# Kernel optimization log

Measured on AMD Instinct MI355X. Metric: run time of the kernel, lower is better.

Reference implementation:

```python
import jax, jax.numpy as jnp
import numpy as np

B, L, A, F = 4096, 12, 768, 4096  # batch, n_layers, d_activations, d_features


def setup_inputs() -> dict:
    key = jax.random.key(0)
    k_x, k_enc, k_dec, k_m, k_s = jax.random.split(key, 5)
    x = jax.random.normal(k_x, (B, L, A), dtype=jnp.float32)
    # Encoder: uniform(-1/sqrt(F), 1/sqrt(F)) per reset_parameters
    enc_thresh = 1.0 / np.sqrt(F)
    W_enc = jax.random.uniform(k_enc, (L, A, F), jnp.float32, -enc_thresh, enc_thresh)
    # Decoder: triangular weights W_i of shape (i+1, F, A), packed along axis 0.
    # Total rows = L*(L+1)//2. uniform(-1/sqrt(A*L), 1/sqrt(A*L)).
    dec_thresh = 1.0 / np.sqrt(A * L)
    n_tri = L * (L + 1) // 2
    W_dec_packed = jax.random.uniform(k_dec, (n_tri, F, A), jnp.float32, -dec_thresh, dec_thresh)
    # JumpReLU threshold per (layer, feature), init 0.03
    theta = jnp.full((L, F), 0.03, dtype=jnp.float32)
    # Dimensionwise input standardizer stats (per layer, per activation dim)
    in_mean = 0.1 * jax.random.normal(k_m, (L, A), dtype=jnp.float32)
    in_std = 1.0 + 0.1 * jax.random.uniform(k_s, (L, A), dtype=jnp.float32)
    return {"x": x, "in_mean": in_mean, "in_std": in_std, "W_enc": W_enc,
            "theta": theta, "W_dec_packed": W_dec_packed}


def reference(x, in_mean, in_std, W_enc, theta, W_dec_packed):
    # Input standardization: (x - mean) / std, broadcast over batch
    sx = (x - in_mean[None]) / in_std[None]                      # [B, L, A]
    # Encoder: per-layer dense projection
    enc = jnp.einsum('bla,laf->blf', sx, W_enc)                  # [B, L, F]
    # JumpReLU: x * (x > theta)
    act = enc * (enc > theta[None]).astype(enc.dtype)            # [B, L, F]
    # Decoder: triangular accumulation. Layer i reads features of layers 0..i
    # with its own weight tensor W_i (slice of the packed triangular buffer).
    n_layers = W_enc.shape[0]
    preds = []
    off = 0
    for i in range(n_layers):
        W_i = W_dec_packed[off:off + i + 1]                      # [i+1, F, A]
        preds.append(jnp.einsum('blf,lfa->ba', act[:, :i + 1], W_i))
        off += i + 1
    logits = jnp.stack(preds, axis=1)                            # [B, L, A]
    # Original forward returns (logits, encoder_out, concat_w_dec); the
    # concat_w_dec list is just a reshape of the decoder params, omitted here.
    return logits, enc
```

## Files before the change

kernel.cpp:

```cpp
#include <hip/hip_runtime.h>
#include <cstdint>
#include <cstddef>

#define B_ 4096
#define L_ 12
#define A_ 768
#define F_ 4096
#define NTRI 78

typedef __bf16 bf16x8 __attribute__((ext_vector_type(8)));
typedef float f32x4 __attribute__((ext_vector_type(4)));
typedef unsigned short u16x4 __attribute__((ext_vector_type(4)));
typedef unsigned short u16x8 __attribute__((ext_vector_type(8)));

__device__ __forceinline__ unsigned short f32_to_bf16(float f) {
  unsigned int u = __float_as_uint(f);
  u += 0x7fffu + ((u >> 16) & 1u);
  return (unsigned short)(u >> 16);
}

__device__ __forceinline__ void gload_lds16(const void* g, void* l) {
  __builtin_amdgcn_global_load_lds(
      (const __attribute__((address_space(1))) void*)g,
      (__attribute__((address_space(3))) void*)l,
      16, 0, 0);
}

__global__ __launch_bounds__(256) void prep_sx(
    const float* __restrict__ x, const float* __restrict__ mean,
    const float* __restrict__ stdv, unsigned short* __restrict__ sx) {
  size_t i4 = (size_t)blockIdx.x * 256 + threadIdx.x;
  size_t e = i4 * 4;
  if (e >= (size_t)B_ * L_ * A_) return;
  unsigned int a = (unsigned int)(e % A_);
  unsigned int t = (unsigned int)(e / A_);
  unsigned int b = t / L_;
  unsigned int l = t % L_;
  float4 xv = *(const float4*)(x + e);
  float4 mv = *(const float4*)(mean + (size_t)l * A_ + a);
  float4 sv = *(const float4*)(stdv + (size_t)l * A_ + a);
  u16x4 o;
  o.x = f32_to_bf16((xv.x - mv.x) / sv.x);
  o.y = f32_to_bf16((xv.y - mv.y) / sv.y);
  o.z = f32_to_bf16((xv.z - mv.z) / sv.z);
  o.w = f32_to_bf16((xv.w - mv.w) / sv.w);
  *(u16x4*)(sx + ((size_t)l * B_ + b) * A_ + a) = o;
}

__global__ __launch_bounds__(256) void transpose_cvt64(
    const float* __restrict__ in, unsigned short* __restrict__ out,
    int R, int C) {
  __shared__ float tile[64][65];
  const float* inz = in + (size_t)blockIdx.z * R * C;
  unsigned short* outz = out + (size_t)blockIdx.z * R * C;
  const int c0 = blockIdx.x * 64, r0 = blockIdx.y * 64;
  const int t = threadIdx.x;
  {
    const int c = (t & 15) * 4;
    const int rb = t >> 4;
#pragma unroll
    for (int q = 0; q < 4; ++q) {
      const int r = rb + q * 16;
      float4 v = *(const float4*)(inz + (size_t)(r0 + r) * C + (c0 + c));
      tile[r][c] = v.x; tile[r][c + 1] = v.y;
      tile[r][c + 2] = v.z; tile[r][c + 3] = v.w;
    }
  }
  __syncthreads();
  {
    const int c = t >> 2;
    const int rb = (t & 3) * 16;
#pragma unroll
    for (int h = 0; h < 2; ++h) {
      u16x8 o;
#pragma unroll
      for (int j = 0; j < 8; ++j) o[j] = f32_to_bf16(tile[rb + h * 8 + j][c]);
      *(u16x8*)(outz + (size_t)(c0 + c) * R + (r0 + rb + h * 8)) = o;
    }
  }
}

template <class KOffA, class KOffB>
__device__ __forceinline__ void gemm_core64(
    int KT, char* AS, char* BS,
    const char* gA0s, const char* gB0s,
    int ldA, int ldB,
    int w, int wr, int wc, int lane,
    KOffA koffA, KOffB koffB, f32x4 (&acc)[8][4]) {
  const int g = lane >> 4;
  const int fr = lane & 15;
  const uint32_t ssr = (uint32_t)((g ^ ((fr >> 1) & 3)) * 16);
  const uint32_t aBase = (uint32_t)(wr * 128 + fr) * 64 + ssr;
  const uint32_t bBase = (uint32_t)(wc * 64 + fr) * 64 + ssr;

  auto stageA = [&](int kt, int h) {
    const uint32_t off = koffA(kt) + (uint32_t)(h * 64);
    char* d = AS + ((kt & 1) << 15) + (h << 14) + (w << 10);
    gload_lds16(gA0s + off, d);
    gload_lds16(gA0s + off + 128u * (uint32_t)ldA, d + 8192);
  };
  auto stageB = [&](int kt, int h) {
    const uint32_t off = koffB(kt) + (uint32_t)(h * 64);
    char* d = BS + ((kt & 1) << 15) + (h << 14) + (w << 10);
    gload_lds16(gB0s + off, d);
    gload_lds16(gB0s + off + 128u * (uint32_t)ldB, d + 8192);
  };

  stageA(0, 0); stageB(0, 0); stageA(0, 1); stageB(0, 1);
  asm volatile("s_waitcnt vmcnt(4)" ::: "memory");
  __builtin_amdgcn_s_barrier();

  bf16x8 bk[4], aA[4], aB[4];
  for (int kt = 0; kt < KT; ++kt) {
    const char* Ab = AS + ((kt & 1) << 15);
    const char* Bb = BS + ((kt & 1) << 15);
    const bool more = (kt + 1 < KT);
#pragma unroll
    for (int ni = 0; ni < 4; ++ni)
      bk[ni] = *(const bf16x8*)(Bb + bBase + ni * 1024);
#pragma unroll
    for (int mi = 0; mi < 4; ++mi)
      aA[mi] = *(const bf16x8*)(Ab + aBase + mi * 1024);
    if (more) stageA(kt + 1, 0);
    asm volatile("" ::: "memory");
    __builtin_amdgcn_s_barrier();
    __builtin_amdgcn_s_setprio(1);
#pragma unroll
    for (int mi = 0; mi < 4; ++mi)
#pragma unroll
      for (int ni = 0; ni < 4; ++ni)
        acc[mi][ni] = __builtin_amdgcn_mfma_f32_16x16x32_bf16(
            aA[mi], bk[ni], acc[mi][ni], 0, 0, 0);
    __builtin_amdgcn_s_setprio(0);
    asm volatile("" ::: "memory");
    __builtin_amdgcn_s_barrier();
#pragma unroll
    for (int mi = 0; mi < 4; ++mi)
      aB[mi] = *(const bf16x8*)(Ab + aBase + (4 + mi) * 1024);
    if (more) stageB(kt + 1, 0);
    asm volatile("" ::: "memory");
    __builtin_amdgcn_s_barrier();
    __builtin_amdgcn_s_setprio(1);
#pragma unroll
    for (int mi = 0; mi < 4; ++mi)
#pragma unroll
      for (int ni = 0; ni < 4; ++ni)
        acc[mi + 4][ni] = __builtin_amdgcn_mfma_f32_16x16x32_bf16(
            aB[mi], bk[ni], acc[mi + 4][ni], 0, 0, 0);
    __builtin_amdgcn_s_setprio(0);
    if (more) { asm volatile("s_waitcnt vmcnt(4)" ::: "memory"); }
    else      { asm volatile("s_waitcnt vmcnt(0)" ::: "memory"); }
    __builtin_amdgcn_s_barrier();
#pragma unroll
    for (int ni = 0; ni < 4; ++ni)
      bk[ni] = *(const bf16x8*)(Bb + 16384 + bBase + ni * 1024);
#pragma unroll
    for (int mi = 0; mi < 4; ++mi)
      aA[mi] = *(const bf16x8*)(Ab + 16384 + aBase + mi * 1024);
    if (more) stageA(kt + 1, 1);
    asm volatile("" ::: "memory");
    __builtin_amdgcn_s_barrier();
    __builtin_amdgcn_s_setprio(1);
#pragma unroll
    for (int mi = 0; mi < 4; ++mi)
#pragma unroll
      for (int ni = 0; ni < 4; ++ni)
        acc[mi][ni] = __builtin_amdgcn_mfma_f32_16x16x32_bf16(
            aA[mi], bk[ni], acc[mi][ni], 0, 0, 0);
    __builtin_amdgcn_s_setprio(0);
    asm volatile("" ::: "memory");
    __builtin_amdgcn_s_barrier();
#pragma unroll
    for (int mi = 0; mi < 4; ++mi)
      aB[mi] = *(const bf16x8*)(Ab + 16384 + aBase + (4 + mi) * 1024);
    if (more) stageB(kt + 1, 1);
    asm volatile("" ::: "memory");
    __builtin_amdgcn_s_barrier();
    __builtin_amdgcn_s_setprio(1);
#pragma unroll
    for (int mi = 0; mi < 4; ++mi)
#pragma unroll
      for (int ni = 0; ni < 4; ++ni)
        acc[mi + 4][ni] = __builtin_amdgcn_mfma_f32_16x16x32_bf16(
            aB[mi], bk[ni], acc[mi + 4][ni], 0, 0, 0);
    __builtin_amdgcn_s_setprio(0);
    if (more) { asm volatile("s_waitcnt vmcnt(4)" ::: "memory"); }
    __builtin_amdgcn_s_barrier();
  }
}

__global__ __launch_bounds__(512, 2) void enc_gemm8(
    const unsigned short* __restrict__ sxT,
    const unsigned short* __restrict__ wT,
    const float* __restrict__ theta,
    float* __restrict__ enc_out,
    unsigned short* __restrict__ act)
{
  extern __shared__ __align__(16) char lds[];
  char* AS = lds;
  char* BS = lds + 65536;
  const int b = blockIdx.x;
  const int wg = (b & 7) * 384 + (b >> 3);
  const int l = wg >> 8;
  const int blk = wg & 255;
  const int m0 = (blk & 15) * 256;
  const int n0 = (blk >> 4) * 256;
  const int tid = threadIdx.x;
  const int w = tid >> 6, lane = tid & 63;
  const int wr = w >> 2, wc = w & 3;
  const int srowS = w * 16 + (lane >> 2);
  const int chnkS = ((lane & 3) ^ ((lane >> 3) & 3)) * 16;

  const char* gA0s = (const char*)sxT +
      ((size_t)l * B_ + m0 + srowS) * (A_ * 2) + chnkS;
  const char* gB0s = (const char*)wT +
      ((size_t)l * F_ + n0 + srowS) * (A_ * 2) + chnkS;

  f32x4 acc[8][4] = {};
  auto koffA = [](int kt) { return (uint32_t)kt * 128u; };
  auto koffB = [](int kt) { return (uint32_t)kt * 128u; };
  gemm_core64(A_ / 64, AS, BS, gA0s, gB0s, A_ * 2, A_ * 2, w, wr, wc, lane,
              koffA, koffB, acc);

  const int g = lane >> 4, fr = lane & 15;
#pragma unroll
  for (int ni = 0; ni < 4; ++ni) {
    const int gcol = n0 + wc * 64 + ni * 16 + fr;
    const float th = theta[(size_t)l * F_ + gcol];
#pragma unroll
    for (int mi = 0; mi < 8; ++mi) {
      const int growb = m0 + wr * 128 + mi * 16 + g * 4;
#pragma unroll
      for (int jj = 0; jj < 4; ++jj) {
        const float v = acc[mi][ni][jj];
        const size_t grow = (size_t)(growb + jj);
        enc_out[(grow * L_ + l) * F_ + gcol] = v;
        act[((size_t)l * B_ + grow) * F_ + gcol] =
            (v > th) ? f32_to_bf16(v) : (unsigned short)0;
      }
    }
  }
}

__global__ __launch_bounds__(512, 2) void dec_gemm8(
    const unsigned short* __restrict__ act,
    const unsigned short* __restrict__ wdecT,
    float* __restrict__ logits)
{
  extern __shared__ __align__(16) char lds[];
  char* AS = lds;
  char* BS = lds + 65536;
  const int b = blockIdx.x;
  const int z = b / 48;
  const int blk = b - z * 48;
  const int i = 11 - z;
  const int m0 = (blk & 15) * 256;
  const int n0 = (blk >> 4) * 256;
  const int triBase = i * (i + 1) / 2;
  const int KT = (i + 1) * 64;
  const int tid = threadIdx.x;
  const int w = tid >> 6, lane = tid & 63;
  const int wr = w >> 2, wc = w & 3;
  const int srowS = w * 16 + (lane >> 2);
  const int chnkS = ((lane & 3) ^ ((lane >> 3) & 3)) * 16;

  const char* gA0s =
      (const char*)act + ((size_t)(m0 + srowS)) * (F_ * 2) + chnkS;
  const char* gB0s = (const char*)wdecT +
      ((size_t)(triBase * A_ + n0 + srowS)) * (F_ * 2) + chnkS;

  f32x4 acc[8][4] = {};
  auto koffA = [](int kt) {
    return (uint32_t)(kt >> 6) * (uint32_t)(B_ * F_ * 2) +
           (uint32_t)(kt & 63) * 128u;
  };
  auto koffB = [](int kt) {
    return (uint32_t)(kt >> 6) * (uint32_t)(A_ * F_ * 2) +
           (uint32_t)(kt & 63) * 128u;
  };
  gemm_core64(KT, AS, BS, gA0s, gB0s, F_ * 2, F_ * 2, w, wr, wc, lane,
              koffA, koffB, acc);

  const int g = lane >> 4, fr = lane & 15;
#pragma unroll
  for (int mi = 0; mi < 8; ++mi) {
    const int growb = m0 + wr * 128 + mi * 16 + g * 4;
#pragma unroll
    for (int ni = 0; ni < 4; ++ni) {
      const int gcol = n0 + wc * 64 + ni * 16 + fr;
#pragma unroll
      for (int jj = 0; jj < 4; ++jj)
        logits[((size_t)(growb + jj) * L_ + i) * A_ + gcol] = acc[mi][ni][jj];
    }
  }
}

extern "C" void kernel_launch(void* const* d_in, const int* in_sizes, int n_in,
                              void* d_out, int out_size, void* d_ws,
                              size_t ws_size, hipStream_t stream) {
  (void)in_sizes; (void)n_in; (void)out_size; (void)ws_size;
  const float* x = (const float*)d_in[0];
  const float* mean = (const float*)d_in[1];
  const float* stdv = (const float*)d_in[2];
  const float* Wenc = (const float*)d_in[3];
  const float* theta = (const float*)d_in[4];
  const float* Wdec = (const float*)d_in[5];

  float* logits = (float*)d_out;
  float* enc = (float*)d_out + (size_t)B_ * L_ * A_;

  char* ws = (char*)d_ws;
  const size_t actBytes = (size_t)L_ * B_ * F_ * 2;
  const size_t sxBytes = (size_t)L_ * B_ * A_ * 2;
  unsigned short* act = (unsigned short*)ws;
  unsigned short* sx = (unsigned short*)(ws + actBytes);
  unsigned short* wencT = (unsigned short*)(ws + actBytes + sxBytes);
  unsigned short* wdecT = (unsigned short*)(ws + actBytes);

  hipFuncSetAttribute((const void*)enc_gemm8,
                      hipFuncAttributeMaxDynamicSharedMemorySize, 131072);
  hipFuncSetAttribute((const void*)dec_gemm8,
                      hipFuncAttributeMaxDynamicSharedMemorySize, 131072);

  prep_sx<<<(B_ * L_ * A_ / 4 + 255) / 256, 256, 0, stream>>>(x, mean, stdv, sx);
  transpose_cvt64<<<dim3(F_ / 64, A_ / 64, L_), 256, 0, stream>>>(
      Wenc, wencT, A_, F_);
  enc_gemm8<<<3072, 512, 131072, stream>>>(sx, wencT, theta, enc, act);
  transpose_cvt64<<<dim3(A_ / 64, F_ / 64, NTRI), 256, 0, stream>>>(
      Wdec, wdecT, F_, A_);
  dec_gemm8<<<576, 512, 131072, stream>>>(act, wdecT, logits);
}
```

Before: 2.856 ms.

## Fold most decoder weight transposes into encoder GEMM launch as interleaved blocks

```diff
diff --git a/kernel.cpp b/kernel.cpp
--- a/kernel.cpp
+++ b/kernel.cpp
@@ -189,18 +189,60 @@
   }
 }
 
-__global__ __launch_bounds__(512, 2) void enc_gemm8(
+__global__ __launch_bounds__(512, 2) void enc_fused(
     const unsigned short* __restrict__ sxT,
     const unsigned short* __restrict__ wT,
     const float* __restrict__ theta,
     float* __restrict__ enc_out,
-    unsigned short* __restrict__ act)
+    unsigned short* __restrict__ act,
+    const float* __restrict__ wdec_in,
+    unsigned short* __restrict__ wdecT_out)
 {
   extern __shared__ __align__(16) char lds[];
+  const int bidx = blockIdx.x;
+  const int grp = bidx / 17;
+  const int rem = bidx - grp * 17;
+
+  if (rem >= 8) {
+    const int tr = grp * 9 + (rem - 8);
+    const int y = tr & 63;
+    const int z = 24 + (tr >> 6);
+    float (*tile)[65] = (float(*)[65])lds;
+    const float* inz = wdec_in + (size_t)z * F_ * A_;
+    unsigned short* outz = wdecT_out + (size_t)z * F_ * A_;
+    const int r0 = y * 64;
+    const int t = threadIdx.x;
+    for (int xq = 0; xq < 12; ++xq) {
+      const int c0 = xq * 64;
+      {
+        const int c = (t & 15) * 4;
+        const int rb = t >> 4;
+#pragma unroll
+        for (int q = 0; q < 2; ++q) {
+          const int r = rb + q * 32;
+          float4 v = *(const float4*)(inz + (size_t)(r0 + r) * A_ + (c0 + c));
+          tile[r][c] = v.x; tile[r][c + 1] = v.y;
+          tile[r][c + 2] = v.z; tile[r][c + 3] = v.w;
+        }
+      }
+      __syncthreads();
+      {
+        const int c = t >> 3;
+        const int rb8 = (t & 7) * 8;
+        u16x8 o;
+#pragma unroll
+        for (int j = 0; j < 8; ++j) o[j] = f32_to_bf16(tile[rb8 + j][c]);
+        *(u16x8*)(outz + (size_t)(c0 + c) * F_ + (r0 + rb8)) = o;
+      }
+      __syncthreads();
+    }
+    return;
+  }
+
   char* AS = lds;
   char* BS = lds + 65536;
-  const int b = blockIdx.x;
-  const int wg = (b & 7) * 384 + (b >> 3);
+  const int e = grp * 8 + rem;
+  const int wg = (e & 7) * 384 + (e >> 3);
   const int l = wg >> 8;
   const int blk = wg & 255;
   const int m0 = (blk & 15) * 256;
@@ -317,7 +359,7 @@
   unsigned short* wencT = (unsigned short*)(ws + actBytes + sxBytes);
   unsigned short* wdecT = (unsigned short*)(ws + actBytes);
 
-  hipFuncSetAttribute((const void*)enc_gemm8,
+  hipFuncSetAttribute((const void*)enc_fused,
                       hipFuncAttributeMaxDynamicSharedMemorySize, 131072);
   hipFuncSetAttribute((const void*)dec_gemm8,
                       hipFuncAttributeMaxDynamicSharedMemorySize, 131072);
@@ -325,8 +367,9 @@
   prep_sx<<<(B_ * L_ * A_ / 4 + 255) / 256, 256, 0, stream>>>(x, mean, stdv, sx);
   transpose_cvt64<<<dim3(F_ / 64, A_ / 64, L_), 256, 0, stream>>>(
       Wenc, wencT, A_, F_);
-  enc_gemm8<<<3072, 512, 131072, stream>>>(sx, wencT, theta, enc, act);
-  transpose_cvt64<<<dim3(A_ / 64, F_ / 64, NTRI), 256, 0, stream>>>(
+  enc_fused<<<6528, 512, 131072, stream>>>(sx, wencT, theta, enc, act,
+                                           Wdec, wdecT);
+  transpose_cvt64<<<dim3(A_ / 64, F_ / 64, 24), 256, 0, stream>>>(
       Wdec, wdecT, F_, A_);
   dec_gemm8<<<576, 512, 131072, stream>>>(act, wdecT, logits);
 }
```

Result: faster. 2.757 ms (-3.5%).
